# Performance work log

Measured on AMD Instinct MI355X. Metric: run time of the kernel, lower is better.

## Reference

```python
import jax, jax.numpy as jnp
import numpy as np

HEADS = 16
EMBED = 1024
HEAD_DIM = EMBED // HEADS


def setup_inputs() -> dict:
    key = jax.random.key(0)
    ks = jax.random.split(key, 11)
    B, S, E = 4, 2048, EMBED
    s = 1.0 / np.sqrt(E)
    return {
        "query": jax.random.normal(ks[0], (B, S, E), jnp.float32),
        "key": jax.random.normal(ks[1], (B, S, E), jnp.float32),
        "value": jax.random.normal(ks[2], (B, S, E), jnp.float32),
        "Wq": jax.random.normal(ks[3], (E, E), jnp.float32) * s,
        "bq": jax.random.normal(ks[4], (E,), jnp.float32) * s,
        "Wk": jax.random.normal(ks[5], (E, E), jnp.float32) * s,
        "bk": jax.random.normal(ks[6], (E,), jnp.float32) * s,
        "Wv": jax.random.normal(ks[7], (E, E), jnp.float32) * s,
        "bv": jax.random.normal(ks[8], (E,), jnp.float32) * s,
        "Wo": jax.random.normal(ks[9], (E, E), jnp.float32) * s,
        "bo": jax.random.normal(ks[10], (E,), jnp.float32) * s,
    }


def reference(query, key, value, Wq, bq, Wk, bk, Wv, bv, Wo, bo):
    B, Sq, E = query.shape
    Sk = key.shape[1]
    H, D = HEADS, HEAD_DIM
    # linear projections (torch Linear: x @ W.T + b)
    q = (query @ Wq.T + bq).reshape(B, Sq, H, D)
    k = (key @ Wk.T + bk).reshape(B, Sk, H, D)
    v = (value @ Wv.T + bv).reshape(B, Sk, H, D)
    scores = jnp.einsum("bqhd,bkhd->bhqk", q, k) / np.sqrt(D).astype(jnp.float32)
    attn = jax.nn.softmax(scores, axis=-1)
    out = jnp.einsum("bhqk,bkhd->bqhd", attn, v).reshape(B, Sq, E)
    # dropout p=0.0 -> identity
    return out @ Wo.T + bo
```

## Files before the change

kernel.cpp:

```cpp
#include <hip/hip_runtime.h>
#include <hip/hip_bf16.h>
#include <stdint.h>

#define BATCH 4
#define SEQ   2048
#define EMB   1024
#define NHEAD 16
#define HDIM  64

typedef __bf16 bf16x8 __attribute__((ext_vector_type(8)));
typedef float  f32x4  __attribute__((ext_vector_type(4)));
typedef float  f32x16 __attribute__((ext_vector_type(16)));

__global__ __launch_bounds__(256) void cvt_f32_bf16(const float* __restrict__ in,
                                                    __bf16* __restrict__ out, int n4) {
  int i = blockIdx.x * 256 + threadIdx.x;
  if (i >= n4) return;
  float4 v = reinterpret_cast<const float4*>(in)[i];
  union { ushort4 u; __bf16 b[4]; } o;
  o.b[0] = (__bf16)v.x; o.b[1] = (__bf16)v.y;
  o.b[2] = (__bf16)v.z; o.b[3] = (__bf16)v.w;
  reinterpret_cast<ushort4*>(out)[i] = o.u;
}

__device__ __forceinline__ void gload_lds16(const void* g, void* l) {
  __builtin_amdgcn_global_load_lds((const uint32_t __attribute__((address_space(1)))*)g,
                                   (uint32_t __attribute__((address_space(3)))*)l, 16, 0, 0);
}

enum { EPI_BF16 = 0, EPI_F32 = 1, EPI_VT = 2 };

template <int MODE>
__global__ __launch_bounds__(256, 2)
void gemm_bt(const __bf16* __restrict__ A, const __bf16* __restrict__ Bt,
             const float* __restrict__ bias, void* __restrict__ Cout,
             int M, int N, int K) {
  __shared__ __bf16 As[128 * 32];
  __shared__ __bf16 Bs[128 * 32];
  const int tid  = threadIdx.x;
  const int wave = tid >> 6, lane = tid & 63;
  const int l4 = lane >> 4, l15 = lane & 15;
  const int row0 = blockIdx.x * 128, col0 = blockIdx.y * 128;
  const int wr = (wave >> 1) * 64, wc = (wave & 1) * 64;

  const int srow = wave * 16 + (lane >> 2);
  const int scol = (lane & 3) * 8;

  f32x4 acc[4][4] = {};

  const __bf16* ga = A  + (size_t)(row0 + srow) * K + scol;
  const __bf16* gb = Bt + (size_t)(col0 + srow) * K + scol;
  char* lA = (char*)As + wave * 1024;
  char* lB = (char*)Bs + wave * 1024;

  for (int k0 = 0; k0 < K; k0 += 32) {
    __syncthreads();
    gload_lds16(ga + k0, lA);
    gload_lds16(ga + k0 + (size_t)64 * K, lA + 4096);
    gload_lds16(gb + k0, lB);
    gload_lds16(gb + k0 + (size_t)64 * K, lB + 4096);
    __syncthreads();

    bf16x8 af[4], bfv[4];
#pragma unroll
    for (int m = 0; m < 4; ++m)
      af[m] = *(const bf16x8*)((const char*)As + (wr + m * 16 + l15) * 64 + l4 * 16);
#pragma unroll
    for (int n = 0; n < 4; ++n)
      bfv[n] = *(const bf16x8*)((const char*)Bs + (wc + n * 16 + l15) * 64 + l4 * 16);
#pragma unroll
    for (int m = 0; m < 4; ++m)
#pragma unroll
      for (int n = 0; n < 4; ++n)
        acc[m][n] = __builtin_amdgcn_mfma_f32_16x16x32_bf16(af[m], bfv[n], acc[m][n], 0, 0, 0);
  }

#pragma unroll
  for (int m = 0; m < 4; ++m) {
    const int r = row0 + wr + m * 16 + l4 * 4;
#pragma unroll
    for (int n = 0; n < 4; ++n) {
      const int c  = col0 + wc + n * 16 + l15;
      const float bb = bias[c];
      if (MODE == EPI_F32) {
        float* C = (float*)Cout;
#pragma unroll
        for (int i = 0; i < 4; ++i) C[(size_t)(r + i) * N + c] = acc[m][n][i] + bb;
      } else if (MODE == EPI_BF16) {
        __bf16* C = (__bf16*)Cout;
#pragma unroll
        for (int i = 0; i < 4; ++i) C[(size_t)(r + i) * N + c] = (__bf16)(acc[m][n][i] + bb);
      } else {
        const int b = r >> 11, s = r & (SEQ - 1);
        const int h = c >> 6, d = c & (HDIM - 1);
        union { ushort4 u; __bf16 x[4]; } o;
#pragma unroll
        for (int i = 0; i < 4; ++i) o.x[i] = (__bf16)(acc[m][n][i] + bb);
        *(ushort4*)((__bf16*)Cout + ((size_t)((b * NHEAD + h) * HDIM + d)) * SEQ + s) = o.u;
      }
    }
  }
}

__device__ __forceinline__ f32x16 mfma32(bf16x8 a, bf16x8 b, f32x16 c) {
  return __builtin_amdgcn_mfma_f32_32x32x16_bf16(a, b, c, 0, 0, 0);
}

__global__ __launch_bounds__(512, 2)
void attn_fwd2(const __bf16* __restrict__ Q, const __bf16* __restrict__ Kk,
               const __bf16* __restrict__ Vt, __bf16* __restrict__ O) {
  __shared__ __bf16 Ks[2][64 * 64];
  __shared__ __bf16 Vs[2][64 * 64];

  const int tid = threadIdx.x;
  const int w = tid >> 6, lane = tid & 63;
  const int l31 = lane & 31, hi = lane >> 5;
  const int bh = blockIdx.x, b = bh >> 4, h = bh & 15;
  const int q0 = blockIdx.y * 256 + w * 32;

  bf16x8 qf[4];
  {
    const __bf16* qb = Q + (size_t)(b * SEQ + q0 + l31) * EMB + h * HDIM + hi * 8;
#pragma unroll
    for (int ks = 0; ks < 4; ++ks) {
      bf16x8 t = *(const bf16x8*)(qb + ks * 16);
#pragma unroll
      for (int j = 0; j < 8; ++j) t[j] = (__bf16)((float)t[j] * 0.125f);
      qf[ks] = t;
    }
  }

  const int srow = w * 8 + (lane >> 3);
  const int sswz = ((lane & 7) * 16) ^ ((srow & 7) << 4);
  const char* kg = (const char*)(Kk + (size_t)(b * SEQ) * EMB + h * HDIM)
                   + (size_t)srow * (EMB * 2) + sswz;
  const char* vg = (const char*)(Vt + (size_t)((b * NHEAD + h) * HDIM) * SEQ)
                   + (size_t)srow * (SEQ * 2) + sswz;

  auto STAGE = [&](int bi, int t) {
    gload_lds16(kg + (size_t)t * (64 * EMB * 2), (char*)&Ks[bi][0] + w * 1024);
    gload_lds16(vg + (size_t)t * 128,            (char*)&Vs[bi][0] + w * 1024);
  };

  f32x16 oacc0 = {}, oacc1 = {};
  float mx = -1e30f, ls = 0.f;
  const int rswz = (l31 & 7) << 4;

  STAGE(0, 0);
  for (int t = 0; t < 32; ++t) {
    const int bi = t & 1;
    if (t < 31) {
      STAGE(bi ^ 1, t + 1);
      asm volatile("s_waitcnt vmcnt(2)" ::: "memory");
    } else {
      asm volatile("s_waitcnt vmcnt(0)" ::: "memory");
    }
    __builtin_amdgcn_s_barrier();
    __builtin_amdgcn_sched_barrier(0);

    f32x16 sc0 = {}, sc1 = {};
    const char* kb = (const char*)&Ks[bi][0];
#pragma unroll
    for (int ks = 0; ks < 4; ++ks) {
      const int o = (ks * 32 + hi * 16) ^ rswz;
      bf16x8 k0 = *(const bf16x8*)(kb + l31 * 128 + o);
      bf16x8 k1 = *(const bf16x8*)(kb + (l31 + 32) * 128 + o);
      sc0 = mfma32(k0, qf[ks], sc0);
      sc1 = mfma32(k1, qf[ks], sc1);
    }

    float pm = sc0[0];
#pragma unroll
    for (int r = 1; r < 16; ++r) pm = fmaxf(pm, sc0[r]);
#pragma unroll
    for (int r = 0; r < 16; ++r) pm = fmaxf(pm, sc1[r]);
    pm = fmaxf(pm, __shfl_xor(pm, 32));
    const float mn = fmaxf(mx, pm);
    const float corr = __expf(mx - mn);
    mx = mn;
    float rs = 0.f;
#pragma unroll
    for (int r = 0; r < 16; ++r) { sc0[r] = __expf(sc0[r] - mn); rs += sc0[r]; }
#pragma unroll
    for (int r = 0; r < 16; ++r) { sc1[r] = __expf(sc1[r] - mn); rs += sc1[r]; }
    rs += __shfl_xor(rs, 32);
    ls = ls * corr + rs;
#pragma unroll
    for (int r = 0; r < 16; ++r) { oacc0[r] *= corr; oacc1[r] *= corr; }

    union Fu { uint32_t w[4]; bf16x8 v; };
    auto pk = [](float a, float b) -> uint32_t {
      union { __bf16 h[2]; uint32_t u; } z;
      z.h[0] = (__bf16)a; z.h[1] = (__bf16)b; return z.u;
    };
    bf16x8 pa[4];
    {
      uint32_t A0 = pk(sc0[0], sc0[1]),  A1 = pk(sc0[2], sc0[3]);
      uint32_t B0 = pk(sc0[4], sc0[5]),  B1 = pk(sc0[6], sc0[7]);
      uint32_t C0 = pk(sc0[8], sc0[9]),  C1 = pk(sc0[10], sc0[11]);
      uint32_t D0 = pk(sc0[12], sc0[13]), D1 = pk(sc0[14], sc0[15]);
      uint32_t sA0 = __shfl_xor((int)A0, 32), sA1 = __shfl_xor((int)A1, 32);
      uint32_t sB0 = __shfl_xor((int)B0, 32), sB1 = __shfl_xor((int)B1, 32);
      uint32_t sC0 = __shfl_xor((int)C0, 32), sC1 = __shfl_xor((int)C1, 32);
      uint32_t sD0 = __shfl_xor((int)D0, 32), sD1 = __shfl_xor((int)D1, 32);
      Fu f0, f1;
      f0.w[0] = hi ? sB0 : A0;  f0.w[1] = hi ? sB1 : A1;
      f0.w[2] = hi ? B0 : sA0;  f0.w[3] = hi ? B1 : sA1;
      f1.w[0] = hi ? sD0 : C0;  f1.w[1] = hi ? sD1 : C1;
      f1.w[2] = hi ? D0 : sC0;  f1.w[3] = hi ? D1 : sC1;
      pa[0] = f0.v; pa[1] = f1.v;
      uint32_t E0 = pk(sc1[0], sc1[1]),  E1 = pk(sc1[2], sc1[3]);
      uint32_t F0 = pk(sc1[4], sc1[5]),  F1 = pk(sc1[6], sc1[7]);
      uint32_t G0 = pk(sc1[8], sc1[9]),  G1 = pk(sc1[10], sc1[11]);
      uint32_t H0 = pk(sc1[12], sc1[13]), H1 = pk(sc1[14], sc1[15]);
      uint32_t sE0 = __shfl_xor((int)E0, 32), sE1 = __shfl_xor((int)E1, 32);
      uint32_t sF0 = __shfl_xor((int)F0, 32), sF1 = __shfl_xor((int)F1, 32);
      uint32_t sG0 = __shfl_xor((int)G0, 32), sG1 = __shfl_xor((int)G1, 32);
      uint32_t sH0 = __shfl_xor((int)H0, 32), sH1 = __shfl_xor((int)H1, 32);
      Fu f2, f3;
      f2.w[0] = hi ? sF0 : E0;  f2.w[1] = hi ? sF1 : E1;
      f2.w[2] = hi ? F0 : sE0;  f2.w[3] = hi ? F1 : sE1;
      f3.w[0] = hi ? sH0 : G0;  f3.w[1] = hi ? sH1 : G1;
      f3.w[2] = hi ? H0 : sG0;  f3.w[3] = hi ? H1 : sG1;
      pa[2] = f2.v; pa[3] = f3.v;
    }

    const char* vb = (const char*)&Vs[bi][0];
#pragma unroll
    for (int ks = 0; ks < 4; ++ks) {
      const int o = (ks * 32 + hi * 16) ^ rswz;
      bf16x8 v0 = *(const bf16x8*)(vb + l31 * 128 + o);
      bf16x8 v1 = *(const bf16x8*)(vb + (l31 + 32) * 128 + o);
      oacc0 = mfma32(v0, pa[ks], oacc0);
      oacc1 = mfma32(v1, pa[ks], oacc1);
    }

    __builtin_amdgcn_s_barrier();
    __builtin_amdgcn_sched_barrier(0);
  }

  const float inv = 1.f / ls;
  __bf16* ob = O + (size_t)(b * SEQ + q0 + l31) * EMB + h * HDIM;
#pragma unroll
  for (int c = 0; c < 4; ++c) {
    union { ushort4 u; __bf16 x[4]; } o0, o1;
#pragma unroll
    for (int i = 0; i < 4; ++i) {
      o0.x[i] = (__bf16)(oacc0[4 * c + i] * inv);
      o1.x[i] = (__bf16)(oacc1[4 * c + i] * inv);
    }
    *(ushort4*)(ob + 8 * c + 4 * hi)      = o0.u;
    *(ushort4*)(ob + 32 + 8 * c + 4 * hi) = o1.u;
  }
}

extern "C" void kernel_launch(void* const* d_in, const int* in_sizes, int n_in,
                              void* d_out, int out_size, void* d_ws, size_t ws_size,
                              hipStream_t stream) {
  const float* query = (const float*)d_in[0];
  const float* key   = (const float*)d_in[1];
  const float* value = (const float*)d_in[2];
  const float* Wq = (const float*)d_in[3]; const float* bq = (const float*)d_in[4];
  const float* Wk = (const float*)d_in[5]; const float* bk = (const float*)d_in[6];
  const float* Wv = (const float*)d_in[7]; const float* bv = (const float*)d_in[8];
  const float* Wo = (const float*)d_in[9]; const float* bo = (const float*)d_in[10];

  char* ws = (char*)d_ws;
  const size_t MB = 1u << 20;
  __bf16* Xb  = (__bf16*)(ws);
  __bf16* Qb  = (__bf16*)(ws + 16 * MB);
  __bf16* Kb  = (__bf16*)(ws + 32 * MB);
  __bf16* Vt  = (__bf16*)(ws + 48 * MB);
  __bf16* Wqb = (__bf16*)(ws + 64 * MB);
  __bf16* Wkb = (__bf16*)(ws + 66 * MB);
  __bf16* Wvb = (__bf16*)(ws + 68 * MB);
  __bf16* Wob = (__bf16*)(ws + 70 * MB);

  const int NE = BATCH * SEQ * EMB;
  const int NW = EMB * EMB;
  const int M = BATCH * SEQ;

  dim3 blk(256);
  dim3 gg(M / 128, EMB / 128);

  cvt_f32_bf16<<<dim3(NW / 4 / 256), blk, 0, stream>>>(Wq, Wqb, NW / 4);
  cvt_f32_bf16<<<dim3(NW / 4 / 256), blk, 0, stream>>>(Wk, Wkb, NW / 4);
  cvt_f32_bf16<<<dim3(NW / 4 / 256), blk, 0, stream>>>(Wv, Wvb, NW / 4);
  cvt_f32_bf16<<<dim3(NW / 4 / 256), blk, 0, stream>>>(Wo, Wob, NW / 4);

  cvt_f32_bf16<<<dim3(NE / 4 / 256), blk, 0, stream>>>(query, Xb, NE / 4);
  gemm_bt<EPI_BF16><<<gg, blk, 0, stream>>>(Xb, Wqb, bq, Qb, M, EMB, EMB);
  cvt_f32_bf16<<<dim3(NE / 4 / 256), blk, 0, stream>>>(key, Xb, NE / 4);
  gemm_bt<EPI_BF16><<<gg, blk, 0, stream>>>(Xb, Wkb, bk, Kb, M, EMB, EMB);
  cvt_f32_bf16<<<dim3(NE / 4 / 256), blk, 0, stream>>>(value, Xb, NE / 4);
  gemm_bt<EPI_VT><<<gg, blk, 0, stream>>>(Xb, Wvb, bv, Vt, M, EMB, EMB);

  attn_fwd2<<<dim3(BATCH * NHEAD, SEQ / 256), dim3(512), 0, stream>>>(Qb, Kb, Vt, Xb);

  gemm_bt<EPI_F32><<<gg, blk, 0, stream>>>(Xb, Wob, bo, d_out, M, EMB, EMB);
}
```

Measured before the change: 383.2 us.

## Batch conversions and QKV GEMMs into single launches, use exp2 softmax with lazy rescale

Merges the four weight conversions and three input conversions into two grid-batched kernels, and runs the Q/K/V projection GEMMs as one launch with blockIdx.z selecting the arguments. Input bf16 buffers are staged in the output buffer and workspace so all three can live at once. In attention, log2(e) is folded into the Q scale and native exp2 replaces __expf. The running max and accumulator rescale are updated only when some lane's new max exceeds the old by more than 8. These cut launch overhead and softmax ALU work, at the cost of runtime epilogue-mode branching in the GEMM and possible precision change from the deferred-max trick.

```diff
diff --git a/kernel.cpp b/kernel.cpp
--- a/kernel.cpp
+++ b/kernel.cpp
@@ -12,29 +12,55 @@
 typedef float  f32x4  __attribute__((ext_vector_type(4)));
 typedef float  f32x16 __attribute__((ext_vector_type(16)));
 
-__global__ __launch_bounds__(256) void cvt_f32_bf16(const float* __restrict__ in,
-                                                    __bf16* __restrict__ out, int n4) {
-  int i = blockIdx.x * 256 + threadIdx.x;
-  if (i >= n4) return;
-  float4 v = reinterpret_cast<const float4*>(in)[i];
-  union { ushort4 u; __bf16 b[4]; } o;
-  o.b[0] = (__bf16)v.x; o.b[1] = (__bf16)v.y;
-  o.b[2] = (__bf16)v.z; o.b[3] = (__bf16)v.w;
-  reinterpret_cast<ushort4*>(out)[i] = o.u;
-}
+extern "C" __device__ float __ocml_native_exp2_f32(float);
 
 __device__ __forceinline__ void gload_lds16(const void* g, void* l) {
   __builtin_amdgcn_global_load_lds((const uint32_t __attribute__((address_space(1)))*)g,
                                    (uint32_t __attribute__((address_space(3)))*)l, 16, 0, 0);
 }
 
+__global__ __launch_bounds__(256) void cvt_inputs(const float* __restrict__ q,
+                                                  const float* __restrict__ k,
+                                                  const float* __restrict__ v,
+                                                  __bf16* xq, __bf16* xk, __bf16* xv, int n4) {
+  const float* in = (blockIdx.y == 0) ? q : (blockIdx.y == 1) ? k : v;
+  __bf16* out     = (blockIdx.y == 0) ? xq : (blockIdx.y == 1) ? xk : xv;
+  int i = blockIdx.x * 256 + threadIdx.x;
+  if (i >= n4) return;
+  float4 t = reinterpret_cast<const float4*>(in)[i];
+  union { ushort4 u; __bf16 b[4]; } o;
+  o.b[0] = (__bf16)t.x; o.b[1] = (__bf16)t.y;
+  o.b[2] = (__bf16)t.z; o.b[3] = (__bf16)t.w;
+  reinterpret_cast<ushort4*>(out)[i] = o.u;
+}
+
+__global__ __launch_bounds__(256) void cvt_weights(const float* w0, const float* w1,
+                                                   const float* w2, const float* w3,
+                                                   __bf16* o0, __bf16* o1,
+                                                   __bf16* o2, __bf16* o3, int n4) {
+  const float* in = (blockIdx.y == 0) ? w0 : (blockIdx.y == 1) ? w1 : (blockIdx.y == 2) ? w2 : w3;
+  __bf16* out     = (blockIdx.y == 0) ? o0 : (blockIdx.y == 1) ? o1 : (blockIdx.y == 2) ? o2 : o3;
+  int i = blockIdx.x * 256 + threadIdx.x;
+  if (i >= n4) return;
+  float4 t = reinterpret_cast<const float4*>(in)[i];
+  union { ushort4 u; __bf16 b[4]; } o;
+  o.b[0] = (__bf16)t.x; o.b[1] = (__bf16)t.y;
+  o.b[2] = (__bf16)t.z; o.b[3] = (__bf16)t.w;
+  reinterpret_cast<ushort4*>(out)[i] = o.u;
+}
+
 enum { EPI_BF16 = 0, EPI_F32 = 1, EPI_VT = 2 };
 
-template <int MODE>
-__global__ __launch_bounds__(256, 2)
-void gemm_bt(const __bf16* __restrict__ A, const __bf16* __restrict__ Bt,
-             const float* __restrict__ bias, void* __restrict__ Cout,
-             int M, int N, int K) {
+struct GArg {
+  const __bf16* A; const __bf16* Bt; const float* bias; void* C; int mode;
+};
+
+__global__ __launch_bounds__(256, 3)
+void gemm97(GArg g0, GArg g1, GArg g2) {
+  GArg g = g0;
+  if (blockIdx.z == 1) g = g1;
+  else if (blockIdx.z == 2) g = g2;
+
   __shared__ __bf16 As[128 * 32];
   __shared__ __bf16 Bs[128 * 32];
   const int tid  = threadIdx.x;
@@ -48,17 +74,17 @@
 
   f32x4 acc[4][4] = {};
 
-  const __bf16* ga = A  + (size_t)(row0 + srow) * K + scol;
-  const __bf16* gb = Bt + (size_t)(col0 + srow) * K + scol;
+  const __bf16* ga = g.A  + (size_t)(row0 + srow) * EMB + scol;
+  const __bf16* gb = g.Bt + (size_t)(col0 + srow) * EMB + scol;
   char* lA = (char*)As + wave * 1024;
   char* lB = (char*)Bs + wave * 1024;
 
-  for (int k0 = 0; k0 < K; k0 += 32) {
+  for (int k0 = 0; k0 < EMB; k0 += 32) {
     __syncthreads();
     gload_lds16(ga + k0, lA);
-    gload_lds16(ga + k0 + (size_t)64 * K, lA + 4096);
+    gload_lds16(ga + k0 + 64 * EMB, lA + 4096);
     gload_lds16(gb + k0, lB);
-    gload_lds16(gb + k0 + (size_t)64 * K, lB + 4096);
+    gload_lds16(gb + k0 + 64 * EMB, lB + 4096);
     __syncthreads();
 
     bf16x8 af[4], bfv[4];
@@ -81,22 +107,22 @@
 #pragma unroll
     for (int n = 0; n < 4; ++n) {
       const int c  = col0 + wc + n * 16 + l15;
-      const float bb = bias[c];
-      if (MODE == EPI_F32) {
-        float* C = (float*)Cout;
-#pragma unroll
-        for (int i = 0; i < 4; ++i) C[(size_t)(r + i) * N + c] = acc[m][n][i] + bb;
-      } else if (MODE == EPI_BF16) {
-        __bf16* C = (__bf16*)Cout;
-#pragma unroll
-        for (int i = 0; i < 4; ++i) C[(size_t)(r + i) * N + c] = (__bf16)(acc[m][n][i] + bb);
+      const float bb = g.bias[c];
+      if (g.mode == EPI_F32) {
+        float* C = (float*)g.C;
+#pragma unroll
+        for (int i = 0; i < 4; ++i) C[(size_t)(r + i) * EMB + c] = acc[m][n][i] + bb;
+      } else if (g.mode == EPI_BF16) {
+        __bf16* C = (__bf16*)g.C;
+#pragma unroll
+        for (int i = 0; i < 4; ++i) C[(size_t)(r + i) * EMB + c] = (__bf16)(acc[m][n][i] + bb);
       } else {
         const int b = r >> 11, s = r & (SEQ - 1);
         const int h = c >> 6, d = c & (HDIM - 1);
         union { ushort4 u; __bf16 x[4]; } o;
 #pragma unroll
         for (int i = 0; i < 4; ++i) o.x[i] = (__bf16)(acc[m][n][i] + bb);
-        *(ushort4*)((__bf16*)Cout + ((size_t)((b * NHEAD + h) * HDIM + d)) * SEQ + s) = o.u;
+        *(ushort4*)((__bf16*)g.C + ((size_t)((b * NHEAD + h) * HDIM + d)) * SEQ + s) = o.u;
       }
     }
   }
@@ -125,7 +151,7 @@
     for (int ks = 0; ks < 4; ++ks) {
       bf16x8 t = *(const bf16x8*)(qb + ks * 16);
 #pragma unroll
-      for (int j = 0; j < 8; ++j) t[j] = (__bf16)((float)t[j] * 0.125f);
+      for (int j = 0; j < 8; ++j) t[j] = (__bf16)((float)t[j] * 0.1803368801111244f);
       qf[ks] = t;
     }
   }
@@ -175,18 +201,27 @@
 #pragma unroll
     for (int r = 0; r < 16; ++r) pm = fmaxf(pm, sc1[r]);
     pm = fmaxf(pm, __shfl_xor(pm, 32));
-    const float mn = fmaxf(mx, pm);
-    const float corr = __expf(mx - mn);
-    mx = mn;
+
+    const bool resc = __any(pm > mx + 8.0f);
+    float corr = 1.0f;
+    if (resc) {
+      const float mn = fmaxf(mx, pm);
+      corr = __ocml_native_exp2_f32(mx - mn);
+      mx = mn;
+    }
     float rs = 0.f;
 #pragma unroll
-    for (int r = 0; r < 16; ++r) { sc0[r] = __expf(sc0[r] - mn); rs += sc0[r]; }
-#pragma unroll
-    for (int r = 0; r < 16; ++r) { sc1[r] = __expf(sc1[r] - mn); rs += sc1[r]; }
+    for (int r = 0; r < 16; ++r) { sc0[r] = __ocml_native_exp2_f32(sc0[r] - mx); rs += sc0[r]; }
+#pragma unroll
+    for (int r = 0; r < 16; ++r) { sc1[r] = __ocml_native_exp2_f32(sc1[r] - mx); rs += sc1[r]; }
     rs += __shfl_xor(rs, 32);
-    ls = ls * corr + rs;
-#pragma unroll
-    for (int r = 0; r < 16; ++r) { oacc0[r] *= corr; oacc1[r] *= corr; }
+    if (resc) {
+      ls = ls * corr + rs;
+#pragma unroll
+      for (int r = 0; r < 16; ++r) { oacc0[r] *= corr; oacc1[r] *= corr; }
+    } else {
+      ls += rs;
+    }
 
     union Fu { uint32_t w[4]; bf16x8 v; };
     auto pk = [](float a, float b) -> uint32_t {
@@ -267,35 +302,34 @@
 
   char* ws = (char*)d_ws;
   const size_t MB = 1u << 20;
-  __bf16* Xb  = (__bf16*)(ws);
+  __bf16* Xq  = (__bf16*)d_out;
+  __bf16* Xk  = (__bf16*)((char*)d_out + 16 * MB);
+  __bf16* Xv  = (__bf16*)(ws);
   __bf16* Qb  = (__bf16*)(ws + 16 * MB);
   __bf16* Kb  = (__bf16*)(ws + 32 * MB);
   __bf16* Vt  = (__bf16*)(ws + 48 * MB);
-  __bf16* Wqb = (__bf16*)(ws + 64 * MB);
-  __bf16* Wkb = (__bf16*)(ws + 66 * MB);
-  __bf16* Wvb = (__bf16*)(ws + 68 * MB);
-  __bf16* Wob = (__bf16*)(ws + 70 * MB);
+  __bf16* Ao  = (__bf16*)(ws + 64 * MB);
+  __bf16* Wqb = (__bf16*)(ws + 80 * MB);
+  __bf16* Wkb = (__bf16*)(ws + 82 * MB);
+  __bf16* Wvb = (__bf16*)(ws + 84 * MB);
+  __bf16* Wob = (__bf16*)(ws + 86 * MB);
 
   const int NE = BATCH * SEQ * EMB;
   const int NW = EMB * EMB;
   const int M = BATCH * SEQ;
 
-  dim3 blk(256);
-  dim3 gg(M / 128, EMB / 128);
-
-  cvt_f32_bf16<<<dim3(NW / 4 / 256), blk, 0, stream>>>(Wq, Wqb, NW / 4);
-  cvt_f32_bf16<<<dim3(NW / 4 / 256), blk, 0, stream>>>(Wk, Wkb, NW / 4);
-  cvt_f32_bf16<<<dim3(NW / 4 / 256), blk, 0, stream>>>(Wv, Wvb, NW / 4);
-  cvt_f32_bf16<<<dim3(NW / 4 / 256), blk, 0, stream>>>(Wo, Wob, NW / 4);
-
-  cvt_f32_bf16<<<dim3(NE / 4 / 256), blk, 0, stream>>>(query, Xb, NE / 4);
-  gemm_bt<EPI_BF16><<<gg, blk, 0, stream>>>(Xb, Wqb, bq, Qb, M, EMB, EMB);
-  cvt_f32_bf16<<<dim3(NE / 4 / 256), blk, 0, stream>>>(key, Xb, NE / 4);
-  gemm_bt<EPI_BF16><<<gg, blk, 0, stream>>>(Xb, Wkb, bk, Kb, M, EMB, EMB);
-  cvt_f32_bf16<<<dim3(NE / 4 / 256), blk, 0, stream>>>(value, Xb, NE / 4);
-  gemm_bt<EPI_VT><<<gg, blk, 0, stream>>>(Xb, Wvb, bv, Vt, M, EMB, EMB);
-
-  attn_fwd2<<<dim3(BATCH * NHEAD, SEQ / 256), dim3(512), 0, stream>>>(Qb, Kb, Vt, Xb);
-
-  gemm_bt<EPI_F32><<<gg, blk, 0, stream>>>(Xb, Wob, bo, d_out, M, EMB, EMB);
-}
+  cvt_weights<<<dim3(NW / 4 / 256, 4), 256, 0, stream>>>(Wq, Wk, Wv, Wo,
+                                                         Wqb, Wkb, Wvb, Wob, NW / 4);
+  cvt_inputs<<<dim3(NE / 4 / 256, 3), 256, 0, stream>>>(query, key, value,
+                                                        Xq, Xk, Xv, NE / 4);
+
+  GArg gq{Xq, Wqb, bq, Qb, EPI_BF16};
+  GArg gk{Xk, Wkb, bk, Kb, EPI_BF16};
+  GArg gv{Xv, Wvb, bv, Vt, EPI_VT};
+  gemm97<<<dim3(M / 128, EMB / 128, 3), 256, 0, stream>>>(gq, gk, gv);
+
+  attn_fwd2<<<dim3(BATCH * NHEAD, SEQ / 256), 512, 0, stream>>>(Qb, Kb, Vt, Ao);
+
+  GArg go{Ao, Wob, bo, d_out, EPI_F32};
+  gemm97<<<dim3(M / 128, EMB / 128, 1), 256, 0, stream>>>(go, go, go);
+}
```

After: 368.6 us. 3.8% less time.
